# Optimization experiments

Measured on AMD Instinct MI355X. Metric: run time of the kernel, lower is better.

The kernel has to match this reference:

```python
import jax, jax.numpy as jnp
import numpy as np

B, C, D, H, W = 2, 64, 16, 16, 16
GROUPS = 32
EPS = 1e-5


def setup_inputs() -> dict:
    key = jax.random.key(0)
    ks = jax.random.split(key, 12)
    xavier = 1.0 / np.sqrt(C)  # xavier_uniform bound ~ sqrt(6/(C+C)) ~ sqrt(3)/sqrt(C); scale fine for testing
    def w(k):
        return jax.random.uniform(k, (C, C), jnp.float32, -xavier, xavier)
    return {
        "x": jax.random.normal(ks[0], (B, C, D, H, W), jnp.float32),
        "Wq": w(ks[1]), "bq": jnp.zeros((C,), jnp.float32),
        "Wk": w(ks[2]), "bk": jnp.zeros((C,), jnp.float32),
        "Wv": w(ks[3]), "bv": jnp.zeros((C,), jnp.float32),
        "Wp": w(ks[4]) * 1e-5, "bp": jnp.zeros((C,), jnp.float32),
        "gamma": jnp.ones((C,), jnp.float32),
        "beta": jnp.zeros((C,), jnp.float32),
    }


def reference(x, Wq, bq, Wk, bk, Wv, bv, Wp, bp, gamma, beta):
    b, c, d, h_, w_ = x.shape
    n = d * h_ * w_
    xf = x.reshape(b, c, n)  # [B,C,N]
    # 1x1 Conv3d == per-position channel matmul
    q = jnp.einsum('oc,bcn->bon', Wq, xf) + bq[:, None]
    k = jnp.einsum('oc,bcn->bon', Wk, xf) + bk[:, None]
    v = jnp.einsum('oc,bcn->bon', Wv, xf) + bv[:, None]
    # qk = q^T k : [B,N,N]; NOTE: no 1/sqrt(C) scaling in the original module
    qk = jnp.einsum('bci,bcj->bij', q, k)
    wgt = jax.nn.softmax(qk, axis=-1)
    # h[b,c,i] = sum_j v[b,c,j] * w[b,i,j]
    hh = jnp.einsum('bcj,bij->bci', v, wgt)
    hh = jnp.einsum('oc,bcn->bon', Wp, hh) + bp[:, None]
    y = xf + hh  # residual BEFORE norm (post-norm layout)
    # GroupNorm(32, C) over (channels_per_group, spatial)
    yg = y.reshape(b, GROUPS, c // GROUPS, n)
    mean = jnp.mean(yg, axis=(2, 3), keepdims=True)
    var = jnp.var(yg, axis=(2, 3), keepdims=True)
    yn = ((yg - mean) * jax.lax.rsqrt(var + EPS)).reshape(b, c, n)
    yn = yn * gamma[:, None] + beta[:, None]
    out = yn * jax.nn.sigmoid(yn)  # Swish
    return out.reshape(b, c, d, h_, w_)
```

## Files before the change

kernel.cpp:

```cpp
#include <hip/hip_runtime.h>
#include <hip/hip_bf16.h>

#define NB 2
#define NC 64
#define NS 4096
#define KS 8

typedef __attribute__((ext_vector_type(8))) short bf16x8;
typedef __attribute__((ext_vector_type(4))) short bf16x4;
typedef __attribute__((ext_vector_type(4))) float f32x4;
typedef __attribute__((ext_vector_type(4))) float float4v;
typedef __attribute__((ext_vector_type(4))) unsigned int u32x4;

static __device__ __forceinline__ short f2bf(float f) {
    union { float f; unsigned u; } c; c.f = f;
    unsigned r = (c.u + 0x7FFFu + ((c.u >> 16) & 1u)) >> 16;
    return (short)r;
}
static __device__ __forceinline__ float bf2f(short s) {
    union { unsigned u; float f; } c; c.u = ((unsigned)(unsigned short)s) << 16;
    return c.f;
}
static __device__ __forceinline__ unsigned pack_trunc(float a, float b) {
    union { float f; unsigned u; } ca, cb; ca.f = a; cb.f = b;
    return (ca.u >> 16) | (cb.u & 0xFFFF0000u);
}

__global__ __launch_bounds__(256) void qkv_proj(
    const float* __restrict__ x,
    const float* __restrict__ Wq, const float* __restrict__ bq,
    const float* __restrict__ Wk, const float* __restrict__ bk,
    const float* __restrict__ Wv, const float* __restrict__ bv,
    short* __restrict__ qT, short* __restrict__ kT, short* __restrict__ vN)
{
    int t    = threadIdx.x;
    int lane = t & 63;
    int wid  = __builtin_amdgcn_readfirstlane(t >> 6);
    int m    = blockIdx.y;
    int och  = wid * 16;
    int pos  = blockIdx.x * 64 + lane;
    int b = pos >> 12;
    int n = pos & (NS - 1);

    const float* W    = (m == 0) ? Wq : (m == 1) ? Wk : Wv;
    const float* bias = (m == 0) ? bq : (m == 1) ? bk : bv;

    float acc[16];
    #pragma unroll
    for (int o = 0; o < 16; ++o) acc[o] = bias[och + o];

    const float* xb = x + (size_t)b * NC * NS + n;
    #pragma unroll 4
    for (int c = 0; c < NC; ++c) {
        float xv = xb[(size_t)c * NS];
        #pragma unroll
        for (int o = 0; o < 16; ++o)
            acc[o] = fmaf(W[(och + o) * NC + c], xv, acc[o]);
    }

    if (m < 2) {
        union U8 { bf16x8 v; short s[8]; } u0, u1;
        #pragma unroll
        for (int o = 0; o < 8; ++o) { u0.s[o] = f2bf(acc[o]); u1.s[o] = f2bf(acc[8 + o]); }
        short* dst = (m == 0 ? qT : kT) + ((size_t)b * NS + n) * NC + och;
        *(bf16x8*)dst       = u0.v;
        *(bf16x8*)(dst + 8) = u1.v;
    } else {
        #pragma unroll
        for (int o = 0; o < 16; ++o)
            vN[((size_t)b * NC + och + o) * NS + n] = f2bf(acc[o]);
    }
}

__global__ __launch_bounds__(512) void flash_attn(
    const short* __restrict__ qT, const short* __restrict__ kT,
    const short* __restrict__ vN, short* __restrict__ Opart,
    float* __restrict__ Mpart, float* __restrict__ Lpart)
{
    int t = threadIdx.x;
    int wid  = t >> 6;
    int lane = t & 63;
    int r = lane & 15;
    int g = lane >> 4;
    int qb = blockIdx.x;
    int ks = blockIdx.y;
    int b  = blockIdx.z;
    int i0 = qb * 128 + wid * 16;

    __shared__ short sK[2][4096];
    __shared__ short sV[2][4096];

    const short* qbp = qT + (size_t)b * NS * NC;
    const short* kbp = kT + (size_t)b * NS * NC;
    const short* vbp = vN + (size_t)b * NC * NS;

    const bf16x8* qrow = (const bf16x8*)(qbp + (size_t)(i0 + r) * NC);
    bf16x8 qf0 = qrow[g];
    bf16x8 qf1 = qrow[4 + g];

    int rt = t >> 3;
    int cl = t & 7;
    int sw = ((cl ^ (rt & 7)) << 3);
    const short* ks_base = kbp + (size_t)rt * NC + sw;
    const short* vs_base = vbp + (size_t)rt * NS + sw;
    short* kdst = &sK[0][0] + ((t >> 6) << 9);
    short* vdst = &sV[0][0] + ((t >> 6) << 9);

    int jbeg = ks * (NS / KS);

    __builtin_amdgcn_global_load_lds((const void*)(ks_base + (size_t)jbeg * NC), (void*)kdst, 16, 0, 0);
    __builtin_amdgcn_global_load_lds((const void*)(vs_base + jbeg),              (void*)vdst, 16, 0, 0);
    __syncthreads();

    f32x4 o_acc[4];
    #pragma unroll
    for (int cc = 0; cc < 4; ++cc) o_acc[cc] = (f32x4){0.f, 0.f, 0.f, 0.f};
    float m_run = -__builtin_inff();
    float l_run = 0.f;

    int bufc = 0;
    for (int it = 0; it < NS / KS / 64; ++it) {
        if (it < NS / KS / 64 - 1) {
            int j1 = jbeg + (it + 1) * 64;
            __builtin_amdgcn_global_load_lds((const void*)(ks_base + (size_t)j1 * NC),
                                             (void*)(kdst + (bufc ^ 1) * 4096), 16, 0, 0);
            __builtin_amdgcn_global_load_lds((const void*)(vs_base + j1),
                                             (void*)(vdst + (bufc ^ 1) * 4096), 16, 0, 0);
        }
        const short* Kt = &sK[bufc][0];
        const short* Vt = &sV[bufc][0];

        f32x4 s[4];
        #pragma unroll
        for (int jj = 0; jj < 4; ++jj) {
            int row = jj * 16 + r;
            int rx = row & 7;
            bf16x8 ka = *(const bf16x8*)(Kt + row * 64 + ((g ^ rx) << 3));
            bf16x8 kb2 = *(const bf16x8*)(Kt + row * 64 + (((4 + g) ^ rx) << 3));
            f32x4 acc = (f32x4){0.f, 0.f, 0.f, 0.f};
            acc = __builtin_amdgcn_mfma_f32_16x16x32_bf16(ka,  qf0, acc, 0, 0, 0);
            acc = __builtin_amdgcn_mfma_f32_16x16x32_bf16(kb2, qf1, acc, 0, 0, 0);
            s[jj] = acc;
        }
        float pmax = -__builtin_inff();
        #pragma unroll
        for (int jj = 0; jj < 4; ++jj)
            #pragma unroll
            for (int e = 0; e < 4; ++e)
                pmax = fmaxf(pmax, s[jj][e]);
        pmax = fmaxf(pmax, __shfl_xor(pmax, 16));
        pmax = fmaxf(pmax, __shfl_xor(pmax, 32));

        if (!__all(pmax - m_run <= 8.f)) {
            float m_new = fmaxf(m_run, pmax);
            float alpha = __expf(m_run - m_new);
            m_run = m_new;
            l_run *= alpha;
            #pragma unroll
            for (int cc = 0; cc < 4; ++cc)
                #pragma unroll
                for (int e = 0; e < 4; ++e)
                    o_acc[cc][e] *= alpha;
        }

        float p[16];
        float lsum = 0.f;
        #pragma unroll
        for (int jj = 0; jj < 4; ++jj)
            #pragma unroll
            for (int e = 0; e < 4; ++e) {
                float pv = __expf(s[jj][e] - m_run);
                p[jj * 4 + e] = pv;
                lsum += pv;
            }
        l_run += lsum;

        union UP { u32x4 u; bf16x8 v; } pf0, pf1;
        #pragma unroll
        for (int e = 0; e < 4; ++e) {
            pf0.u[e] = pack_trunc(p[2 * e],     p[2 * e + 1]);
            pf1.u[e] = pack_trunc(p[8 + 2 * e], p[9 + 2 * e]);
        }
        #pragma unroll
        for (int cc = 0; cc < 4; ++cc) {
            int row = cc * 16 + r;
            int rxs = (row & 7) << 3;
            const short* vr = Vt + row * 64;
            union UV { bf16x8 v; bf16x4 h[2]; };
            UV vf;
            vf.h[0] = *(const bf16x4*)(vr + ((4 * g) ^ rxs));
            vf.h[1] = *(const bf16x4*)(vr + ((4 * g + 16) ^ rxs));
            o_acc[cc] = __builtin_amdgcn_mfma_f32_16x16x32_bf16(vf.v, pf0.v, o_acc[cc], 0, 0, 0);
            vf.h[0] = *(const bf16x4*)(vr + ((4 * g + 32) ^ rxs));
            vf.h[1] = *(const bf16x4*)(vr + ((4 * g + 48) ^ rxs));
            o_acc[cc] = __builtin_amdgcn_mfma_f32_16x16x32_bf16(vf.v, pf1.v, o_acc[cc], 0, 0, 0);
        }
        __syncthreads();
        bufc ^= 1;
    }

    float lt = l_run + __shfl_xor(l_run, 16);
    lt += __shfl_xor(lt, 32);

    size_t pb = (size_t)(ks * NB + b);
    #pragma unroll
    for (int cc = 0; cc < 4; ++cc)
        #pragma unroll
        for (int e = 0; e < 4; ++e)
            Opart[(pb * NC + cc * 16 + g * 4 + e) * NS + i0 + r] = f2bf(o_acc[cc][e]);
    if (lane < 16) {
        Mpart[pb * NS + i0 + r] = m_run;
        Lpart[pb * NS + i0 + r] = lt;
    }
}

__global__ __launch_bounds__(256) void flash_combine(
    const short* __restrict__ Opart, const float* __restrict__ Mpart,
    const float* __restrict__ Lpart, float* __restrict__ h)
{
    int idx = blockIdx.x * 256 + threadIdx.x;
    int n0 = (idx & 511) * 8;
    int c  = (idx >> 9) & 63;
    int b  = idx >> 15;

    float M[8], L[8], O[8];
    #pragma unroll
    for (int j = 0; j < 8; ++j) { M[j] = -__builtin_inff(); L[j] = 0.f; O[j] = 0.f; }

    #pragma unroll
    for (int k = 0; k < KS; ++k) {
        size_t pb = (size_t)(k * NB + b);
        const float* mp = Mpart + pb * NS + n0;
        const float* lp = Lpart + pb * NS + n0;
        float4v ma = *(const float4v*)mp;
        float4v mb = *(const float4v*)(mp + 4);
        float4v la = *(const float4v*)lp;
        float4v lb = *(const float4v*)(lp + 4);
        union U8 { bf16x8 v; short s[8]; } op;
        op.v = *(const bf16x8*)(Opart + (pb * NC + c) * NS + n0);
        #pragma unroll
        for (int j = 0; j < 8; ++j) {
            float mk = (j < 4) ? ma[j] : mb[j - 4];
            float lk = (j < 4) ? la[j] : lb[j - 4];
            float Mn = fmaxf(M[j], mk);
            float sc = __expf(M[j] - Mn);
            float a  = __expf(mk - Mn);
            L[j] = L[j] * sc + a * lk;
            O[j] = O[j] * sc + a * bf2f(op.s[j]);
            M[j] = Mn;
        }
    }
    float* hb = h + ((size_t)b * NC + c) * NS + n0;
    float4v o0, o1;
    #pragma unroll
    for (int j = 0; j < 4; ++j) {
        o0[j] = O[j] / L[j];
        o1[j] = O[4 + j] / L[4 + j];
    }
    *(float4v*)hb       = o0;
    *(float4v*)(hb + 4) = o1;
}

__global__ __launch_bounds__(256) void out_proj(
    const float* __restrict__ x, const float* __restrict__ Wp,
    const float* __restrict__ bp, const float* __restrict__ h,
    float* __restrict__ y)
{
    int t    = threadIdx.x;
    int lane = t & 63;
    int wid  = __builtin_amdgcn_readfirstlane(t >> 6);
    int och  = wid * 16;
    int pos  = blockIdx.x * 64 + lane;
    int b = pos >> 12;
    int n = pos & (NS - 1);

    float acc[16];
    #pragma unroll
    for (int o = 0; o < 16; ++o) acc[o] = bp[och + o];
    const float* hb = h + (size_t)b * NC * NS + n;
    #pragma unroll 4
    for (int c = 0; c < NC; ++c) {
        float hv = hb[(size_t)c * NS];
        #pragma unroll
        for (int o = 0; o < 16; ++o)
            acc[o] = fmaf(Wp[(och + o) * NC + c], hv, acc[o]);
    }
    const float* xb = x + (size_t)b * NC * NS + n;
    float* yb = y + (size_t)b * NC * NS + n;
    #pragma unroll
    for (int o = 0; o < 16; ++o)
        yb[(size_t)(och + o) * NS] = acc[o] + xb[(size_t)(och + o) * NS];
}

__global__ __launch_bounds__(1024) void groupnorm_swish(
    const float* __restrict__ y, const float* __restrict__ gamma,
    const float* __restrict__ beta, float* __restrict__ out)
{
    int t  = threadIdx.x;
    int bg = blockIdx.x;
    int b  = bg >> 5;
    int gr = bg & 31;
    size_t base = ((size_t)b * NC + gr * 2) * NS;

    float4v v0 = *(const float4v*)(y + base + t * 8);
    float4v v1 = *(const float4v*)(y + base + t * 8 + 4);
    float s = 0.f, s2 = 0.f;
    #pragma unroll
    for (int i = 0; i < 4; ++i) {
        s += v0[i] + v1[i];
        s2 += v0[i] * v0[i] + v1[i] * v1[i];
    }
    #pragma unroll
    for (int off = 32; off; off >>= 1) {
        s  += __shfl_xor(s, off);
        s2 += __shfl_xor(s2, off);
    }
    __shared__ float ls[16], ls2[16];
    int wid = t >> 6, lane = t & 63;
    if (lane == 0) { ls[wid] = s; ls2[wid] = s2; }
    __syncthreads();
    float st = 0.f, s2t = 0.f;
    #pragma unroll
    for (int w = 0; w < 16; ++w) { st += ls[w]; s2t += ls2[w]; }
    float mean = st * (1.f / 8192.f);
    float var  = s2t * (1.f / 8192.f) - mean * mean;
    float rstd = rsqrtf(var + 1e-5f);
    float gg = (t < 512) ? gamma[gr * 2] : gamma[gr * 2 + 1];
    float bb = (t < 512) ? beta[gr * 2]  : beta[gr * 2 + 1];
    float4v o0, o1;
    #pragma unroll
    for (int i = 0; i < 4; ++i) {
        float yn = (v0[i] - mean) * rstd * gg + bb;
        o0[i] = yn / (1.f + __expf(-yn));
        float yn1 = (v1[i] - mean) * rstd * gg + bb;
        o1[i] = yn1 / (1.f + __expf(-yn1));
    }
    *(float4v*)(out + base + t * 8)     = o0;
    *(float4v*)(out + base + t * 8 + 4) = o1;
}

extern "C" void kernel_launch(void* const* d_in, const int* in_sizes, int n_in,
                              void* d_out, int out_size, void* d_ws, size_t ws_size,
                              hipStream_t stream)
{
    const float* x     = (const float*)d_in[0];
    const float* Wq    = (const float*)d_in[1];
    const float* bq    = (const float*)d_in[2];
    const float* Wk    = (const float*)d_in[3];
    const float* bk    = (const float*)d_in[4];
    const float* Wv    = (const float*)d_in[5];
    const float* bv    = (const float*)d_in[6];
    const float* Wp    = (const float*)d_in[7];
    const float* bp    = (const float*)d_in[8];
    const float* gamma = (const float*)d_in[9];
    const float* beta  = (const float*)d_in[10];
    float* out = (float*)d_out;

    char* ws = (char*)d_ws;
    short* qT    = (short*)(ws);
    short* kT    = (short*)(ws + (1u << 20));
    short* vN    = (short*)(ws + (2u << 20));
    short* Opart = (short*)(ws + (3u << 20));
    float* Mpart = (float*)(ws + (11u << 20));
    float* Lpart = (float*)(ws + (11u << 20) + (256u << 10));
    float* h     = (float*)(ws + (12u << 20));
    float* y     = (float*)(ws + (14u << 20));

    qkv_proj<<<dim3(128, 3), 256, 0, stream>>>(x, Wq, bq, Wk, bk, Wv, bv, qT, kT, vN);
    flash_attn<<<dim3(32, KS, 2), 512, 0, stream>>>(qT, kT, vN, Opart, Mpart, Lpart);
    flash_combine<<<256, 256, 0, stream>>>(Opart, Mpart, Lpart, h);
    out_proj<<<128, 256, 0, stream>>>(x, Wp, bp, h, y);
    groupnorm_swish<<<64, 1024, 0, stream>>>(y, gamma, beta, out);
}
```

Before: 128.4 us.

## Fuse combine, output projection and groupnorm-swish into one cooperative kernel

Replaces the three tail kernels (split-K combine, out_proj, groupnorm_swish) with a single cooperative kernel. It merges the partial flash outputs straight into LDS, runs the projection plus residual in registers, and writes per-block group statistics. A grid-wide sync then lets every block finish GroupNorm and Swish without storing h or y to global memory. This removes two launches and the h/y round trips, at the cost of a grid barrier, a cooperative launch, and strided per-element Opart loads in place of vectorized ones.

```diff
diff --git a/kernel.cpp b/kernel.cpp
--- a/kernel.cpp
+++ b/kernel.cpp
@@ -1,5 +1,8 @@
 #include <hip/hip_runtime.h>
 #include <hip/hip_bf16.h>
+#include <hip/hip_cooperative_groups.h>
+
+namespace cg = cooperative_groups;
 
 #define NB 2
 #define NC 64
@@ -135,7 +138,7 @@
         for (int jj = 0; jj < 4; ++jj) {
             int row = jj * 16 + r;
             int rx = row & 7;
-            bf16x8 ka = *(const bf16x8*)(Kt + row * 64 + ((g ^ rx) << 3));
+            bf16x8 ka  = *(const bf16x8*)(Kt + row * 64 + ((g ^ rx) << 3));
             bf16x8 kb2 = *(const bf16x8*)(Kt + row * 64 + (((4 + g) ^ rx) << 3));
             f32x4 acc = (f32x4){0.f, 0.f, 0.f, 0.f};
             acc = __builtin_amdgcn_mfma_f32_16x16x32_bf16(ka,  qf0, acc, 0, 0, 0);
@@ -214,129 +217,108 @@
     }
 }
 
-__global__ __launch_bounds__(256) void flash_combine(
+__global__ __launch_bounds__(256) void fused_tail(
     const short* __restrict__ Opart, const float* __restrict__ Mpart,
-    const float* __restrict__ Lpart, float* __restrict__ h)
-{
-    int idx = blockIdx.x * 256 + threadIdx.x;
-    int n0 = (idx & 511) * 8;
-    int c  = (idx >> 9) & 63;
-    int b  = idx >> 15;
-
-    float M[8], L[8], O[8];
-    #pragma unroll
-    for (int j = 0; j < 8; ++j) { M[j] = -__builtin_inff(); L[j] = 0.f; O[j] = 0.f; }
-
-    #pragma unroll
-    for (int k = 0; k < KS; ++k) {
-        size_t pb = (size_t)(k * NB + b);
-        const float* mp = Mpart + pb * NS + n0;
-        const float* lp = Lpart + pb * NS + n0;
-        float4v ma = *(const float4v*)mp;
-        float4v mb = *(const float4v*)(mp + 4);
-        float4v la = *(const float4v*)lp;
-        float4v lb = *(const float4v*)(lp + 4);
-        union U8 { bf16x8 v; short s[8]; } op;
-        op.v = *(const bf16x8*)(Opart + (pb * NC + c) * NS + n0);
-        #pragma unroll
-        for (int j = 0; j < 8; ++j) {
-            float mk = (j < 4) ? ma[j] : mb[j - 4];
-            float lk = (j < 4) ? la[j] : lb[j - 4];
-            float Mn = fmaxf(M[j], mk);
-            float sc = __expf(M[j] - Mn);
-            float a  = __expf(mk - Mn);
-            L[j] = L[j] * sc + a * lk;
-            O[j] = O[j] * sc + a * bf2f(op.s[j]);
-            M[j] = Mn;
-        }
-    }
-    float* hb = h + ((size_t)b * NC + c) * NS + n0;
-    float4v o0, o1;
-    #pragma unroll
-    for (int j = 0; j < 4; ++j) {
-        o0[j] = O[j] / L[j];
-        o1[j] = O[4 + j] / L[4 + j];
-    }
-    *(float4v*)hb       = o0;
-    *(float4v*)(hb + 4) = o1;
-}
-
-__global__ __launch_bounds__(256) void out_proj(
-    const float* __restrict__ x, const float* __restrict__ Wp,
-    const float* __restrict__ bp, const float* __restrict__ h,
-    float* __restrict__ y)
+    const float* __restrict__ Lpart, const float* __restrict__ x,
+    const float* __restrict__ Wp, const float* __restrict__ bp,
+    const float* __restrict__ gamma, const float* __restrict__ beta,
+    float* __restrict__ stats, float* __restrict__ out)
 {
     int t    = threadIdx.x;
     int lane = t & 63;
     int wid  = __builtin_amdgcn_readfirstlane(t >> 6);
-    int och  = wid * 16;
-    int pos  = blockIdx.x * 64 + lane;
-    int b = pos >> 12;
-    int n = pos & (NS - 1);
+    int c0   = wid * 16;
+    int blk  = blockIdx.x;
+    int pos  = blk * 64 + lane;
+    int b    = pos >> 12;
+    int n    = pos & (NS - 1);
+
+    __shared__ float h_lds[64][65];
+
+    float mk[KS], lk[KS];
+    #pragma unroll
+    for (int k = 0; k < KS; ++k) {
+        size_t pb = (size_t)(k * NB + b);
+        mk[k] = Mpart[pb * NS + n];
+        lk[k] = Lpart[pb * NS + n];
+    }
+    float Mt = mk[0];
+    #pragma unroll
+    for (int k = 1; k < KS; ++k) Mt = fmaxf(Mt, mk[k]);
+    float a[KS];
+    float Lt = 0.f;
+    #pragma unroll
+    for (int k = 0; k < KS; ++k) { a[k] = __expf(mk[k] - Mt); Lt += a[k] * lk[k]; }
+    float invL = 1.f / Lt;
+    #pragma unroll
+    for (int o = 0; o < 16; ++o) {
+        int c = c0 + o;
+        float hv = 0.f;
+        #pragma unroll
+        for (int k = 0; k < KS; ++k)
+            hv = fmaf(a[k], bf2f(Opart[((size_t)(k * NB + b) * NC + c) * NS + n]), hv);
+        h_lds[c][lane] = hv * invL;
+    }
+    __syncthreads();
 
     float acc[16];
     #pragma unroll
-    for (int o = 0; o < 16; ++o) acc[o] = bp[och + o];
-    const float* hb = h + (size_t)b * NC * NS + n;
+    for (int o = 0; o < 16; ++o) acc[o] = bp[c0 + o];
     #pragma unroll 4
     for (int c = 0; c < NC; ++c) {
-        float hv = hb[(size_t)c * NS];
+        float hv = h_lds[c][lane];
         #pragma unroll
         for (int o = 0; o < 16; ++o)
-            acc[o] = fmaf(Wp[(och + o) * NC + c], hv, acc[o]);
+            acc[o] = fmaf(Wp[(c0 + o) * NC + c], hv, acc[o]);
     }
     const float* xb = x + (size_t)b * NC * NS + n;
-    float* yb = y + (size_t)b * NC * NS + n;
     #pragma unroll
     for (int o = 0; o < 16; ++o)
-        yb[(size_t)(och + o) * NS] = acc[o] + xb[(size_t)(och + o) * NS];
-}
-
-__global__ __launch_bounds__(1024) void groupnorm_swish(
-    const float* __restrict__ y, const float* __restrict__ gamma,
-    const float* __restrict__ beta, float* __restrict__ out)
-{
-    int t  = threadIdx.x;
-    int bg = blockIdx.x;
-    int b  = bg >> 5;
-    int gr = bg & 31;
-    size_t base = ((size_t)b * NC + gr * 2) * NS;
-
-    float4v v0 = *(const float4v*)(y + base + t * 8);
-    float4v v1 = *(const float4v*)(y + base + t * 8 + 4);
-    float s = 0.f, s2 = 0.f;
-    #pragma unroll
-    for (int i = 0; i < 4; ++i) {
-        s += v0[i] + v1[i];
-        s2 += v0[i] * v0[i] + v1[i] * v1[i];
-    }
-    #pragma unroll
-    for (int off = 32; off; off >>= 1) {
-        s  += __shfl_xor(s, off);
-        s2 += __shfl_xor(s2, off);
-    }
-    __shared__ float ls[16], ls2[16];
-    int wid = t >> 6, lane = t & 63;
-    if (lane == 0) { ls[wid] = s; ls2[wid] = s2; }
-    __syncthreads();
-    float st = 0.f, s2t = 0.f;
-    #pragma unroll
-    for (int w = 0; w < 16; ++w) { st += ls[w]; s2t += ls2[w]; }
-    float mean = st * (1.f / 8192.f);
-    float var  = s2t * (1.f / 8192.f) - mean * mean;
-    float rstd = rsqrtf(var + 1e-5f);
-    float gg = (t < 512) ? gamma[gr * 2] : gamma[gr * 2 + 1];
-    float bb = (t < 512) ? beta[gr * 2]  : beta[gr * 2 + 1];
-    float4v o0, o1;
-    #pragma unroll
-    for (int i = 0; i < 4; ++i) {
-        float yn = (v0[i] - mean) * rstd * gg + bb;
-        o0[i] = yn / (1.f + __expf(-yn));
-        float yn1 = (v1[i] - mean) * rstd * gg + bb;
-        o1[i] = yn1 / (1.f + __expf(-yn1));
-    }
-    *(float4v*)(out + base + t * 8)     = o0;
-    *(float4v*)(out + base + t * 8 + 4) = o1;
+        acc[o] += xb[(size_t)(c0 + o) * NS];
+
+    float* st = stats + (((size_t)b * 64 + (blk & 63)) * 32) * 2;
+    #pragma unroll
+    for (int gq = 0; gq < 8; ++gq) {
+        float s  = acc[2 * gq] + acc[2 * gq + 1];
+        float s2 = acc[2 * gq] * acc[2 * gq] + acc[2 * gq + 1] * acc[2 * gq + 1];
+        #pragma unroll
+        for (int off = 32; off; off >>= 1) {
+            s  += __shfl_xor(s, off);
+            s2 += __shfl_xor(s2, off);
+        }
+        if (lane == 0) {
+            st[(8 * wid + gq) * 2 + 0] = s;
+            st[(8 * wid + gq) * 2 + 1] = s2;
+        }
+    }
+    __threadfence();
+    cg::this_grid().sync();
+
+    float mean_[8], rstd_[8];
+    const float* sb = stats + ((size_t)b * 64 * 32) * 2;
+    #pragma unroll
+    for (int gq = 0; gq < 8; ++gq) {
+        int g = 8 * wid + gq;
+        float s  = sb[((size_t)lane * 32 + g) * 2 + 0];
+        float s2 = sb[((size_t)lane * 32 + g) * 2 + 1];
+        #pragma unroll
+        for (int off = 32; off; off >>= 1) {
+            s  += __shfl_xor(s, off);
+            s2 += __shfl_xor(s2, off);
+        }
+        float mean = s * (1.f / 8192.f);
+        float var  = s2 * (1.f / 8192.f) - mean * mean;
+        mean_[gq] = mean;
+        rstd_[gq] = rsqrtf(var + 1e-5f);
+    }
+
+    float* ob = out + (size_t)b * NC * NS + n;
+    #pragma unroll
+    for (int o = 0; o < 16; ++o) {
+        int gq = o >> 1;
+        float yn = (acc[o] - mean_[gq]) * rstd_[gq] * gamma[c0 + o] + beta[c0 + o];
+        ob[(size_t)(c0 + o) * NS] = yn / (1.f + __expf(-yn));
+    }
 }
 
 extern "C" void kernel_launch(void* const* d_in, const int* in_sizes, int n_in,
@@ -363,12 +345,14 @@
     short* Opart = (short*)(ws + (3u << 20));
     float* Mpart = (float*)(ws + (11u << 20));
     float* Lpart = (float*)(ws + (11u << 20) + (256u << 10));
-    float* h     = (float*)(ws + (12u << 20));
-    float* y     = (float*)(ws + (14u << 20));
+    float* stats = (float*)(ws + (12u << 20));
 
     qkv_proj<<<dim3(128, 3), 256, 0, stream>>>(x, Wq, bq, Wk, bk, Wv, bv, qT, kT, vN);
     flash_attn<<<dim3(32, KS, 2), 512, 0, stream>>>(qT, kT, vN, Opart, Mpart, Lpart);
-    flash_combine<<<256, 256, 0, stream>>>(Opart, Mpart, Lpart, h);
-    out_proj<<<128, 256, 0, stream>>>(x, Wp, bp, h, y);
-    groupnorm_swish<<<64, 1024, 0, stream>>>(y, gamma, beta, out);
-}
+
+    void* args[] = { (void*)&Opart, (void*)&Mpart, (void*)&Lpart, (void*)&x,
+                     (void*)&Wp, (void*)&bp, (void*)&gamma, (void*)&beta,
+                     (void*)&stats, (void*)&out };
+    hipLaunchCooperativeKernel((const void*)fused_tail, dim3(128), dim3(256),
+                               args, 0, stream);
+}
```

Result: slower. 168.5 us (+31.2%).
